# Kernel tuning notes

Measured on AMD Instinct MI355X. Metric: run time of the kernel, lower is better.

The kernel has to match this reference:

```python
import jax, jax.numpy as jnp
import numpy as np


def setup_inputs() -> dict:
    key = jax.random.key(0)
    ks = jax.random.split(key, 12)
    L, B, T, E, H = 8, 256, 8, 1024, 1024
    w_scale = 1.0 / np.sqrt(E + H)  # keep gates out of saturation (mimics Linear init scale)
    inp = {
        "x": jax.random.normal(ks[0], (B, T, E), dtype=jnp.float32),
        "h0": jax.random.normal(ks[1], (L, B, H), dtype=jnp.float32),
        "c0": jax.random.normal(ks[2], (L, B, H), dtype=jnp.float32),
        "Wu": jax.random.normal(ks[3], (L, E + H, H), dtype=jnp.float32) * w_scale,
        "bu": jax.random.normal(ks[4], (L, H), dtype=jnp.float32) * w_scale,
        "Wf": jax.random.normal(ks[5], (L, E + H, H), dtype=jnp.float32) * w_scale,
        "bf": jax.random.normal(ks[6], (L, H), dtype=jnp.float32) * w_scale,
        "Wo": jax.random.normal(ks[7], (L, E + H, H), dtype=jnp.float32) * w_scale,
        "bo": jax.random.normal(ks[8], (L, H), dtype=jnp.float32) * w_scale,
        "Wc": jax.random.normal(ks[9], (L, E + H, H), dtype=jnp.float32) * w_scale,
        "bc": jax.random.normal(ks[10], (L, H), dtype=jnp.float32) * w_scale,
    }
    return inp


def reference(x, h0, c0, Wu, bu, Wf, bf, Wo, bo, Wc, bc):
    # x: [B,T,E]; h0,c0: [L,B,H]; W*: [L,E+H,H]; b*: [L,H]
    # Faithful to source: num_cells layers, time loop over first num_cells steps (T == L here).
    L = h0.shape[0]
    h = jnp.transpose(h0, (1, 0, 2))  # [B,L,H]
    c = jnp.transpose(c0, (1, 0, 2))

    def step(carry, xt):  # xt: [B,E]
        h, c = carry
        inp = xt
        hs, cs = [], []
        for l in range(L):
            zh = jnp.concatenate([inp, h[:, l]], axis=-1)  # [B, E+H]
            u = jax.nn.sigmoid(zh @ Wu[l] + bu[l])
            f = jax.nn.sigmoid(zh @ Wf[l] + bf[l])
            o = jax.nn.sigmoid(zh @ Wo[l] + bo[l])
            c_tilde = jnp.tanh(zh @ Wc[l] + bc[l])
            c_new = f * c[:, l] + u * c_tilde
            h_new = o * jnp.tanh(c_new)
            hs.append(h_new)
            cs.append(c_new)
            inp = h_new
        h = jnp.stack(hs, axis=1)
        c = jnp.stack(cs, axis=1)
        return (h, c), (h_new, c_new)  # emit top-layer h_t, c_t

    (_, _), (hs, cs) = jax.lax.scan(step, (h, c), jnp.transpose(x, (1, 0, 2)))
    hidden_states = jnp.transpose(hs, (1, 0, 2))  # [B,T,H]
    memory_states = jnp.transpose(cs, (1, 0, 2))
    h_t = hidden_states[:, -1:, :]  # [B,1,H], matches torch slice-shape
    c_t = memory_states[:, -1:, :]
    return hidden_states, memory_states, h_t, c_t
```

## Files before the change

### kernel.cpp

```cpp
#include <hip/hip_runtime.h>
#include <hip/hip_bf16.h>

#define B_ 256
#define T_ 8
#define E_ 1024
#define H_ 1024
#define L_ 8
#define KD 2048
#define ND 4096

#define BM 256
#define BN 128
#define BK 64
#define ABYTES 32768
#define BUFBYTES 49152
#define NT (KD / BK)

typedef __bf16 bf16x8 __attribute__((ext_vector_type(8)));
typedef float floatx4 __attribute__((ext_vector_type(4)));

__device__ __forceinline__ float sigm(float x) { return 1.f / (1.f + __expf(-x)); }
__device__ __forceinline__ float tanh_(float x) { return 1.f - 2.f / (__expf(2.f * x) + 1.f); }

__device__ __forceinline__ void async16(const void* g, void* l) {
    __builtin_amdgcn_global_load_lds(
        (const __attribute__((address_space(1))) void*)g,
        (__attribute__((address_space(3))) void*)l, 16, 0, 0);
}

__global__ __launch_bounds__(256) void prep_weights(
    const float* __restrict__ Wu, const float* __restrict__ Wf,
    const float* __restrict__ Wo, const float* __restrict__ Wc,
    __hip_bfloat16* __restrict__ WT)
{
    __shared__ float sm[64][33];
    int bid = blockIdx.x;
    int jt = bid & 31;
    int kt = (bid >> 5) & 31;
    int g  = (bid >> 10) & 3;
    int l  = bid >> 12;
    const float* src = (g == 0) ? Wu : (g == 1) ? Wf : (g == 2) ? Wo : Wc;
    int tid = threadIdx.x;
    int jl = tid & 31;
    int kl0 = tid >> 5;
#pragma unroll
    for (int r = 0; r < 8; ++r) {
        int kl = r * 8 + kl0;
        sm[kl][jl] = src[((size_t)(l * KD + kt * 64 + kl)) * 1024 + jt * 32 + jl];
    }
    __syncthreads();
    int jw = tid >> 3;
    int kc = (tid & 7) * 8;
    bf16x8 v;
#pragma unroll
    for (int i = 0; i < 8; ++i)
        v[i] = (__bf16)sm[kc + i][jw];
    size_t n = (size_t)(jt * 32 + jw) * 4 + g;
    *(bf16x8*)&WT[((size_t)l * ND + n) * KD + kt * 64 + kc] = v;
}

__global__ __launch_bounds__(256) void prep_misc(
    const float* __restrict__ x,  const float* __restrict__ h0,
    const float* __restrict__ c0,
    const float* __restrict__ bu, const float* __restrict__ bfv,
    const float* __restrict__ bo, const float* __restrict__ bc,
    __hip_bfloat16* __restrict__ xbf, __hip_bfloat16* __restrict__ hb0,
    float* __restrict__ cbuf, float* __restrict__ bcat)
{
    size_t i = (size_t)blockIdx.x * 256 + threadIdx.x;
    const size_t NX = (size_t)B_ * T_ * E_;
    const size_t NH = (size_t)L_ * B_ * H_;
    if (i < NX) {
        xbf[i] = __float2bfloat16(x[i]);
    } else if (i < NX + NH) {
        size_t j = i - NX; hb0[j] = __float2bfloat16(h0[j]);
    } else if (i < NX + 2 * NH) {
        size_t j = i - NX - NH; cbuf[j] = c0[j];
    } else if (i < NX + 2 * NH + (size_t)L_ * ND) {
        size_t j = i - NX - 2 * NH;
        int l = (int)(j >> 12); int n = (int)(j & 4095);
        int jj = n >> 2; int g = n & 3;
        const float* bs = (g == 0) ? bu : (g == 1) ? bfv : (g == 2) ? bo : bc;
        bcat[j] = bs[l * 1024 + jj];
    }
}

__global__ __launch_bounds__(512) void lstm_step(
    int d, int tmin,
    const __hip_bfloat16* __restrict__ xbf,
    const __hip_bfloat16* __restrict__ WT,
    const float* __restrict__ bcat,
    __hip_bfloat16* __restrict__ hb0,
    __hip_bfloat16* __restrict__ hb1,
    float* __restrict__ cbuf,
    float* __restrict__ out)
{
    __shared__ __align__(16) char smraw[3][BUFBYTES];

    int cell = blockIdx.x >> 5;
    int nb   = blockIdx.x & 31;
    int t = tmin + cell;
    int l = d - t;

    const __hip_bfloat16* hread  = (t & 1) ? hb1 : hb0;
    __hip_bfloat16*       hwrite = (t & 1) ? hb0 : hb1;

    const __hip_bfloat16* A1; int sA1;
    if (l == 0) { A1 = xbf + (size_t)t * E_;               sA1 = T_ * E_; }
    else        { A1 = hwrite + (size_t)(l - 1) * B_ * H_; sA1 = H_; }
    const __hip_bfloat16* A2 = hread + (size_t)l * B_ * H_;
    const __hip_bfloat16* Bbase = WT + ((size_t)l * ND + (size_t)nb * BN) * KD;

    int tid  = threadIdx.x;
    int lane = tid & 63;
    int wid  = tid >> 6;
    int wm = (wid & 3) * 64;
    int wn = (wid >> 2) * 64;
    int lr   = lane & 15;
    int quad = lane >> 4;

    int srow = tid >> 3;
    int c    = (tid & 7) ^ (srow & 7);
    const __hip_bfloat16* pA1[4];
    const __hip_bfloat16* pA2[4];
    const __hip_bfloat16* pB[2];
#pragma unroll
    for (int s = 0; s < 4; ++s) {
        int row = s * 64 + srow;
        pA1[s] = A1 + (size_t)row * sA1 + c * 8;
        pA2[s] = A2 + (size_t)row * H_ + c * 8 - E_;
    }
#pragma unroll
    for (int s = 0; s < 2; ++s) {
        int row = s * 64 + srow;
        pB[s] = Bbase + (size_t)row * KD + c * 8;
    }
    int ldsWaveOff = wid * 1024;

    auto stage = [&](int k0, int buf) {
        char* dst = smraw[buf];
        bool first = (k0 < E_);
#pragma unroll
        for (int s = 0; s < 4; ++s) {
            const __hip_bfloat16* g = (first ? pA1[s] : pA2[s]) + k0;
            async16(g, dst + s * 8192 + ldsWaveOff);
        }
#pragma unroll
        for (int s = 0; s < 2; ++s) {
            async16(pB[s] + k0, dst + ABYTES + s * 8192 + ldsWaveOff);
        }
    };

    floatx4 acc[4][4];
    floatx4 zero = {0.f, 0.f, 0.f, 0.f};
#pragma unroll
    for (int mi = 0; mi < 4; ++mi)
#pragma unroll
        for (int ni = 0; ni < 4; ++ni) acc[mi][ni] = zero;

    stage(0 * BK, 0);
    stage(1 * BK, 1);
    stage(2 * BK, 2);
    asm volatile("s_waitcnt vmcnt(12)" ::: "memory");
    __builtin_amdgcn_sched_barrier(0);
    __builtin_amdgcn_s_barrier();

    for (int kt = 0; kt < NT; ++kt) {
        int cur = kt % 3;
        const __hip_bfloat16* sm  = (const __hip_bfloat16*)smraw[cur];
        const __hip_bfloat16* smB = sm + ABYTES / 2;

#pragma unroll
        for (int ks = 0; ks < 2; ++ks) {
            int xo = (((ks * 4 + quad) ^ (lr & 7)) * 8);
            bf16x8 af[4], bfr[4];
#pragma unroll
            for (int mi = 0; mi < 4; ++mi)
                af[mi] = *(const bf16x8*)&sm[(wm + mi * 16 + lr) * 64 + xo];
#pragma unroll
            for (int ni = 0; ni < 4; ++ni)
                bfr[ni] = *(const bf16x8*)&smB[(wn + ni * 16 + lr) * 64 + xo];
            asm volatile("s_waitcnt lgkmcnt(0)" ::: "memory");
            __builtin_amdgcn_sched_barrier(0);
            __builtin_amdgcn_s_setprio(1);
#pragma unroll
            for (int mi = 0; mi < 4; ++mi)
#pragma unroll
                for (int ni = 0; ni < 4; ++ni)
                    acc[mi][ni] = __builtin_amdgcn_mfma_f32_16x16x32_bf16(
                        af[mi], bfr[ni], acc[mi][ni], 0, 0, 0);
            __builtin_amdgcn_s_setprio(0);
        }

        __builtin_amdgcn_sched_barrier(0);
        __builtin_amdgcn_s_barrier();

        if (kt + 3 < NT) stage((kt + 3) * BK, cur);

        if (kt < NT - 1) {
            if (kt + 3 < NT)      { asm volatile("s_waitcnt vmcnt(12)" ::: "memory"); }
            else if (kt + 2 < NT) { asm volatile("s_waitcnt vmcnt(6)"  ::: "memory"); }
            else                  { asm volatile("s_waitcnt vmcnt(0)"  ::: "memory"); }
            __builtin_amdgcn_sched_barrier(0);
            __builtin_amdgcn_s_barrier();
        }
    }

    float* outH  = out;
    float* outC  = out + (size_t)B_ * T_ * H_;
    float* outHt = out + 2 * (size_t)B_ * T_ * H_;
    float* outCt = outHt + (size_t)B_ * H_;
    auto sC = (float(*)[BN + 4])smraw[0];

    for (int q = 0; q < 4; ++q) {
        __syncthreads();
        if ((wid & 3) == q) {
#pragma unroll
            for (int mi = 0; mi < 4; ++mi)
#pragma unroll
                for (int ni = 0; ni < 4; ++ni)
#pragma unroll
                    for (int r = 0; r < 4; ++r)
                        sC[mi * 16 + quad * 4 + r][wn + ni * 16 + lr] = acc[mi][ni][r];
        }
        __syncthreads();
#pragma unroll
        for (int s = 0; s < 4; ++s) {
            int p = tid + s * 512;
            int r  = p >> 5;
            int jj = p & 31;
            float4 v  = *(float4*)&sC[r][jj * 4];
            float4 bb = *(const float4*)&bcat[(size_t)l * ND + nb * BN + jj * 4];
            float u  = sigm(v.x + bb.x);
            float f  = sigm(v.y + bb.y);
            float o  = sigm(v.z + bb.z);
            float ct = tanh_(v.w + bb.w);
            int b = q * 64 + r;
            int j = nb * 32 + jj;
            size_t ci = ((size_t)l * B_ + b) * H_ + j;
            float cn = f * cbuf[ci] + u * ct;
            cbuf[ci] = cn;
            float hn = o * tanh_(cn);
            hwrite[ci] = __float2bfloat16(hn);
            if (l == L_ - 1) {
                size_t oi = ((size_t)b * T_ + t) * H_ + j;
                outH[oi] = hn;
                outC[oi] = cn;
                if (t == T_ - 1) {
                    outHt[(size_t)b * H_ + j] = hn;
                    outCt[(size_t)b * H_ + j] = cn;
                }
            }
        }
    }
}

extern "C" void kernel_launch(void* const* d_in, const int* in_sizes, int n_in,
                              void* d_out, int out_size, void* d_ws, size_t ws_size,
                              hipStream_t stream)
{
    const float* x   = (const float*)d_in[0];
    const float* h0  = (const float*)d_in[1];
    const float* c0  = (const float*)d_in[2];
    const float* Wu  = (const float*)d_in[3];
    const float* bu  = (const float*)d_in[4];
    const float* Wf  = (const float*)d_in[5];
    const float* bfv = (const float*)d_in[6];
    const float* Wo  = (const float*)d_in[7];
    const float* bo  = (const float*)d_in[8];
    const float* Wc  = (const float*)d_in[9];
    const float* bc  = (const float*)d_in[10];
    float* out = (float*)d_out;

    char* ws = (char*)d_ws;
    __hip_bfloat16* WT   = (__hip_bfloat16*)(ws);
    float*          bcat = (float*)(ws + 134217728);
    __hip_bfloat16* xbf  = (__hip_bfloat16*)(ws + 134348800);
    __hip_bfloat16* hb0  = (__hip_bfloat16*)(ws + 138543104);
    __hip_bfloat16* hb1  = (__hip_bfloat16*)(ws + 142737408);
    float*          cbuf = (float*)(ws + 146931712);

    hipLaunchKernelGGL(prep_weights, dim3(32768), dim3(256), 0, stream,
                       Wu, Wf, Wo, Wc, WT);
    size_t n2 = (size_t)2097152 * 3 + (size_t)L_ * ND;
    hipLaunchKernelGGL(prep_misc, dim3((unsigned)((n2 + 255) / 256)), dim3(256), 0, stream,
                       x, h0, c0, bu, bfv, bo, bc, xbf, hb0, cbuf, bcat);

    for (int dg = 0; dg <= (T_ - 1) + (L_ - 1); ++dg) {
        int tmin = dg > L_ - 1 ? dg - (L_ - 1) : 0;
        int tmax = dg < T_ - 1 ? dg : T_ - 1;
        int nc = tmax - tmin + 1;
        hipLaunchKernelGGL(lstm_step, dim3(nc * 32), dim3(512), 0, stream,
                           dg, tmin, xbf, WT, bcat, hb0, hb1, cbuf, out);
    }
}
```

Baseline: 969.9 us.

## Restructure GEMM main loop pipeline and vectorize weight prep loads

The LSTM step GEMM loop now keeps two tiles in flight instead of three. It issues the next tile's async load midway through the k-step, after the first half's LDS reads, and splits each k-tile into two explicitly barriered halves. The weight conversion kernel is split into four per-gate launches and reads the fp32 source with float4 loads instead of scalar loads. The goal is better overlap of global loads with MFMA work and higher bandwidth in the prep transpose, at the cost of a shallower prefetch depth and extra barriers per k-step.

```diff
diff --git a/kernel.cpp b/kernel.cpp
--- a/kernel.cpp
+++ b/kernel.cpp
@@ -28,25 +28,25 @@
         (__attribute__((address_space(3))) void*)l, 16, 0, 0);
 }
 
-__global__ __launch_bounds__(256) void prep_weights(
-    const float* __restrict__ Wu, const float* __restrict__ Wf,
-    const float* __restrict__ Wo, const float* __restrict__ Wc,
-    __hip_bfloat16* __restrict__ WT)
+__global__ __launch_bounds__(256) void prep_weights_g(
+    const float* __restrict__ src, __hip_bfloat16* __restrict__ WT, int g)
 {
     __shared__ float sm[64][33];
     int bid = blockIdx.x;
     int jt = bid & 31;
     int kt = (bid >> 5) & 31;
-    int g  = (bid >> 10) & 3;
-    int l  = bid >> 12;
-    const float* src = (g == 0) ? Wu : (g == 1) ? Wf : (g == 2) ? Wo : Wc;
+    int l  = bid >> 10;
     int tid = threadIdx.x;
-    int jl = tid & 31;
-    int kl0 = tid >> 5;
-#pragma unroll
-    for (int r = 0; r < 8; ++r) {
-        int kl = r * 8 + kl0;
-        sm[kl][jl] = src[((size_t)(l * KD + kt * 64 + kl)) * 1024 + jt * 32 + jl];
+    int j4  = tid & 7;
+    int kl0 = tid >> 3;
+#pragma unroll
+    for (int r = 0; r < 2; ++r) {
+        int kl = kl0 + r * 32;
+        float4 v = *(const float4*)&src[((size_t)(l * KD + kt * 64 + kl)) * 1024 + jt * 32 + j4 * 4];
+        sm[kl][j4 * 4 + 0] = v.x;
+        sm[kl][j4 * 4 + 1] = v.y;
+        sm[kl][j4 * 4 + 2] = v.z;
+        sm[kl][j4 * 4 + 3] = v.w;
     }
     __syncthreads();
     int jw = tid >> 3;
@@ -160,19 +160,16 @@
 
     stage(0 * BK, 0);
     stage(1 * BK, 1);
-    stage(2 * BK, 2);
-    asm volatile("s_waitcnt vmcnt(12)" ::: "memory");
-    __builtin_amdgcn_sched_barrier(0);
+    asm volatile("s_waitcnt vmcnt(6)" ::: "memory");
     __builtin_amdgcn_s_barrier();
 
     for (int kt = 0; kt < NT; ++kt) {
-        int cur = kt % 3;
+        const int cur = kt % 3;
         const __hip_bfloat16* sm  = (const __hip_bfloat16*)smraw[cur];
         const __hip_bfloat16* smB = sm + ABYTES / 2;
 
-#pragma unroll
-        for (int ks = 0; ks < 2; ++ks) {
-            int xo = (((ks * 4 + quad) ^ (lr & 7)) * 8);
+        {
+            int xo = ((quad ^ (lr & 7)) * 8);
             bf16x8 af[4], bfr[4];
 #pragma unroll
             for (int mi = 0; mi < 4; ++mi)
@@ -180,8 +177,9 @@
 #pragma unroll
             for (int ni = 0; ni < 4; ++ni)
                 bfr[ni] = *(const bf16x8*)&smB[(wn + ni * 16 + lr) * 64 + xo];
+            if (kt + 2 < NT) stage((kt + 2) * BK, (kt + 2) % 3);
+            __builtin_amdgcn_s_barrier();
             asm volatile("s_waitcnt lgkmcnt(0)" ::: "memory");
-            __builtin_amdgcn_sched_barrier(0);
             __builtin_amdgcn_s_setprio(1);
 #pragma unroll
             for (int mi = 0; mi < 4; ++mi)
@@ -190,18 +188,32 @@
                     acc[mi][ni] = __builtin_amdgcn_mfma_f32_16x16x32_bf16(
                         af[mi], bfr[ni], acc[mi][ni], 0, 0, 0);
             __builtin_amdgcn_s_setprio(0);
-        }
-
-        __builtin_amdgcn_sched_barrier(0);
-        __builtin_amdgcn_s_barrier();
-
-        if (kt + 3 < NT) stage((kt + 3) * BK, cur);
-
-        if (kt < NT - 1) {
-            if (kt + 3 < NT)      { asm volatile("s_waitcnt vmcnt(12)" ::: "memory"); }
-            else if (kt + 2 < NT) { asm volatile("s_waitcnt vmcnt(6)"  ::: "memory"); }
-            else                  { asm volatile("s_waitcnt vmcnt(0)"  ::: "memory"); }
-            __builtin_amdgcn_sched_barrier(0);
+            __builtin_amdgcn_s_barrier();
+        }
+
+        {
+            int xo = (((4 + quad) ^ (lr & 7)) * 8);
+            bf16x8 af[4], bfr[4];
+#pragma unroll
+            for (int mi = 0; mi < 4; ++mi)
+                af[mi] = *(const bf16x8*)&sm[(wm + mi * 16 + lr) * 64 + xo];
+#pragma unroll
+            for (int ni = 0; ni < 4; ++ni)
+                bfr[ni] = *(const bf16x8*)&smB[(wn + ni * 16 + lr) * 64 + xo];
+            __builtin_amdgcn_s_barrier();
+            asm volatile("s_waitcnt lgkmcnt(0)" ::: "memory");
+            __builtin_amdgcn_s_setprio(1);
+#pragma unroll
+            for (int mi = 0; mi < 4; ++mi)
+#pragma unroll
+                for (int ni = 0; ni < 4; ++ni)
+                    acc[mi][ni] = __builtin_amdgcn_mfma_f32_16x16x32_bf16(
+                        af[mi], bfr[ni], acc[mi][ni], 0, 0, 0);
+            __builtin_amdgcn_s_setprio(0);
+            if (kt < NT - 1) {
+                if (kt + 2 < NT) { asm volatile("s_waitcnt vmcnt(6)" ::: "memory"); }
+                else             { asm volatile("s_waitcnt vmcnt(0)" ::: "memory"); }
+            }
             __builtin_amdgcn_s_barrier();
         }
     }
@@ -280,8 +292,10 @@
     __hip_bfloat16* hb1  = (__hip_bfloat16*)(ws + 142737408);
     float*          cbuf = (float*)(ws + 146931712);
 
-    hipLaunchKernelGGL(prep_weights, dim3(32768), dim3(256), 0, stream,
-                       Wu, Wf, Wo, Wc, WT);
+    hipLaunchKernelGGL(prep_weights_g, dim3(8192), dim3(256), 0, stream, Wu, WT, 0);
+    hipLaunchKernelGGL(prep_weights_g, dim3(8192), dim3(256), 0, stream, Wf, WT, 1);
+    hipLaunchKernelGGL(prep_weights_g, dim3(8192), dim3(256), 0, stream, Wo, WT, 2);
+    hipLaunchKernelGGL(prep_weights_g, dim3(8192), dim3(256), 0, stream, Wc, WT, 3);
     size_t n2 = (size_t)2097152 * 3 + (size_t)L_ * ND;
     hipLaunchKernelGGL(prep_misc, dim3((unsigned)((n2 + 255) / 256)), dim3(256), 0, stream,
                        x, h0, c0, bu, bfv, bo, bc, xbf, hb0, cbuf, bcat);
```

Result: no change. 953.5 us (-1.7%).
